# Kernel optimization log

Hardware: AMD Instinct MI355X
Metric: run time of the kernel (lower is better)

Reference implementation:

```python
import jax, jax.numpy as jnp
import numpy as np

NUM_ROUTING = 3


def squash(t, axis=-1):
    # scale * t / ||t||, scale = ||t||^2 / (1 + ||t||^2)  (matches torch code exactly)
    norm = jnp.sum(t * t, axis=axis, keepdims=True)
    return (norm / (1.0 + norm)) * t / jnp.sqrt(norm)


def setup_inputs() -> dict:
    key = jax.random.key(0)
    k1, k2 = jax.random.split(key)
    x = jax.random.normal(k1, (512, 8, 1152), dtype=jnp.float32)      # [B, in_unit, in_channel]
    W = jax.random.normal(k2, (1, 1152, 10, 16, 8), dtype=jnp.float32)  # [1, C, U, unit_size, in_unit]
    return {"x": x, "W": W}


def reference(x, W):
    B = x.shape[0]
    # x.transpose(1,2): [B, C, I];  u_hat = W @ x  -> [B, C, U, O]  (O = unit_size)
    xt = jnp.transpose(x, (0, 2, 1))
    u_hat = jnp.einsum('cuoi,bci->bcuo', W[0], xt)
    # routing logits b_ij, shared across batch: [C, U]
    b = jnp.zeros(u_hat.shape[1:3], dtype=u_hat.dtype)
    v = None
    for _ in range(NUM_ROUTING):
        c = jax.nn.softmax(b, axis=1)                       # softmax over num_unit dim
        s = jnp.einsum('cu,bcuo->buo', c, u_hat)            # sum over in_channel
        v = squash(s, axis=-1)                              # squash over unit_size
        agree = jnp.einsum('bcuo,buo->cu', u_hat, v) / B    # mean over batch
        b = b + agree
    # torch returns v_j.squeeze(1) with trailing singleton -> [B, U, O, 1]
    return v[..., None]
```

## Files before the change

kernel.cpp:

```cpp
#include <hip/hip_runtime.h>
#include <math.h>

#define B_ 512
#define C_ 1152
#define U_ 10
#define O_ 16
#define I_ 8
#define K_ 9216
#define UO_ 160
#define NBLK 256
#define NTHR 1024

typedef short bf16x8 __attribute__((ext_vector_type(8)));
typedef float f32x4 __attribute__((ext_vector_type(4)));
typedef unsigned short u16x8v __attribute__((ext_vector_type(8)));
typedef unsigned long long u64t;

__device__ __attribute__((aligned(16))) unsigned short g_xb2[B_*K_];
__device__ __attribute__((aligned(16))) unsigned short g_xT2[K_*B_];
__device__ __attribute__((aligned(16))) unsigned short g_Wc[3][C_*1280];
__device__ __attribute__((aligned(16))) unsigned g_vT32[2][UO_*B_/2];
__device__ float g_b[C_*U_];
__device__ unsigned g_gen;
__device__ unsigned g_arrive[NBLK];

__device__ __forceinline__ unsigned short f2bf(float f) {
    unsigned u = __builtin_bit_cast(unsigned, f);
    unsigned r = (u + 0x7FFFu + ((u >> 16) & 1u)) >> 16;
    return (unsigned short)r;
}

__device__ __forceinline__ void st_sys16(unsigned short* p, u16x8v v) {
    union { u16x8v v; u64t q[2]; } u; u.v = v;
    __hip_atomic_store((u64t*)p,     u.q[0], __ATOMIC_RELAXED, __HIP_MEMORY_SCOPE_SYSTEM);
    __hip_atomic_store(((u64t*)p)+1, u.q[1], __ATOMIC_RELAXED, __HIP_MEMORY_SCOPE_SYSTEM);
}

__global__ __launch_bounds__(256) void k_prep(const float* __restrict__ x,
                                              const float* __restrict__ W) {
    __shared__ unsigned short lds[32*256];
    int task = blockIdx.x, tid = threadIdx.x;
    if (task < 576) {
        int b0 = (task & 15) * 32;
        int c0 = (task >> 4) * 32;
        int li = tid >> 5, lc = tid & 31;
        for (int rep = 0; rep < 32; rep++) {
            float v = x[(b0+rep)*K_ + li*1152 + c0 + lc];
            lds[rep*256 + ((lc*8+li) ^ ((rep&31)<<3))] = f2bf(v);
        }
        __syncthreads();
        {
            int b = tid >> 3, part = tid & 7;
            int swz = (b&31) << 3;
            const u16x8v* lv = (const u16x8v*)lds;
            u16x8v* ov = (u16x8v*)(g_xb2 + (b0+b)*K_ + c0*8 + part*32);
            #pragma unroll
            for (int g = 0; g < 4; g++)
                ov[g] = lv[(b*256 + ((part*32 + g*8) ^ swz)) >> 3];
        }
        for (int p = 0; p < 8; p++) {
            int r = p*32 + (tid>>3);
            int bp = (tid&7)*4;
            ushort4 o;
            unsigned short* po = (unsigned short*)&o;
            #pragma unroll
            for (int q = 0; q < 4; q++) {
                int b = bp + q;
                po[q] = lds[b*256 + (r ^ ((b&31)<<3))];
            }
            *(ushort4*)(g_xT2 + (c0*8 + r)*B_ + b0 + bp) = o;
        }
    } else {
        int base = (task - 576) * 8192;
        for (int j = 0; j < 8; j++) {
            float4 v = *(const float4*)(W + base + j*1024 + tid*4);
            ushort4 o;
            o.x = f2bf(0.1f*v.x); o.y = f2bf(0.1f*v.y);
            o.z = f2bf(0.1f*v.z); o.w = f2bf(0.1f*v.w);
            *(ushort4*)(&g_Wc[0][0] + base + j*1024 + tid*4) = o;
        }
    }
}

struct TBsh { float agg[2][U_]; float cws[2][U_]; };
union ShMem {
    float red[16][16][32];
    TBsh tb[4];
};

__device__ __forceinline__ void gbar(unsigned target) {
    __syncthreads();
    if (threadIdx.x == 0)
        __hip_atomic_store(&g_arrive[blockIdx.x], target,
                           __ATOMIC_RELAXED, __HIP_MEMORY_SCOPE_SYSTEM);
    if (blockIdx.x == 0) {
        long spins = 0;
        for (;;) {
            int ok = 1;
            if (threadIdx.x < NBLK) {
                unsigned a = __hip_atomic_load(&g_arrive[threadIdx.x],
                                               __ATOMIC_RELAXED, __HIP_MEMORY_SCOPE_SYSTEM);
                ok = (int)(a - target) >= 0;
            }
            if (__syncthreads_count(ok) == NTHR) break;
            __builtin_amdgcn_s_sleep(4);
            if (++spins > (1L << 17)) break;
        }
        if (threadIdx.x == 0)
            __hip_atomic_store(&g_gen, target, __ATOMIC_RELAXED, __HIP_MEMORY_SCOPE_SYSTEM);
    }
    if (threadIdx.x == 0) {
        long spins = 0;
        while ((int)(__hip_atomic_load(&g_gen, __ATOMIC_RELAXED, __HIP_MEMORY_SCOPE_SYSTEM) - target) < 0) {
            __builtin_amdgcn_s_sleep(8);
            if (++spins > (1L << 18)) break;
        }
    }
    __syncthreads();
}

__device__ void ph_s(const unsigned short* __restrict__ Wcr, unsigned* vtw,
                     float* __restrict__ out, int bid, int tid, ShMem& sh) {
    if (bid < 160) {
        int lane = tid & 63, w = tid >> 6;
        int mt = bid & 31, nt = bid >> 5;
        int m0 = mt*16, n0 = nt*32;
        int ra = lane & 15;
        const unsigned short* pa  = g_xb2 + (m0+ra)*K_ + w*576 + (lane>>4)*8;
        const unsigned short* pb0 = Wcr + (w*72 + (lane>>4))*1280 + (n0+ra)*8;
        const unsigned short* pb1 = pb0 + 128;
        f32x4 acc0 = {0.f,0.f,0.f,0.f};
        f32x4 acc1 = {0.f,0.f,0.f,0.f};
        #pragma unroll 6
        for (int s = 0; s < 18; s++) {
            bf16x8 a  = *(const bf16x8*)pa;
            bf16x8 b0 = *(const bf16x8*)pb0;
            bf16x8 b1 = *(const bf16x8*)pb1;
            acc0 = __builtin_amdgcn_mfma_f32_16x16x32_bf16(a, b0, acc0, 0, 0, 0);
            acc1 = __builtin_amdgcn_mfma_f32_16x16x32_bf16(a, b1, acc1, 0, 0, 0);
            pa += 32; pb0 += 5120; pb1 += 5120;
        }
        int row = (lane>>4)*4, col = lane & 15;
        #pragma unroll
        for (int r = 0; r < 4; r++) {
            sh.red[w][row+r][col]    = acc0[r];
            sh.red[w][row+r][col+16] = acc1[r];
        }
        __syncthreads();
        if (tid < 256) {
            int bp = tid >> 5;
            int u  = (tid >> 4) & 1;
            int o  = tid & 15;
            int col2 = u*16 + o;
            float t0 = 0.f, t1 = 0.f;
            #pragma unroll
            for (int ww = 0; ww < 16; ww++) {
                t0 += sh.red[ww][2*bp][col2];
                t1 += sh.red[ww][2*bp+1][col2];
            }
            float n0s = t0*t0, n1s = t1*t1;
            #pragma unroll
            for (int m = 1; m < 16; m <<= 1) {
                n0s += __shfl_xor(n0s, m);
                n1s += __shfl_xor(n1s, m);
            }
            float f0 = n0s / ((1.f + n0s) * sqrtf(n0s));
            float f1 = n1s / ((1.f + n1s) * sqrtf(n1s));
            float v0 = t0*f0, v1 = t1*f1;
            int ug = nt*2 + u;
            int bg = m0 + 2*bp;
            if (vtw) {
                unsigned pack = (unsigned)f2bf(v0) | ((unsigned)f2bf(v1) << 16);
                __hip_atomic_store(&vtw[((ug*16+o)*B_ + bg) >> 1], pack,
                                   __ATOMIC_RELAXED, __HIP_MEMORY_SCOPE_SYSTEM);
            } else {
                out[(bg*10 + ug)*16 + o]       = v0;
                out[((bg+1)*10 + ug)*16 + o]   = v1;
            }
        }
        __syncthreads();
    }
}

__device__ void ph_tb(const float* __restrict__ W, const unsigned* vtr,
                      unsigned short* Wcw, int first, int bid, int tid, ShMem& sh) {
    int lane = tid & 63, lw = (tid >> 6) & 3, g = tid >> 8;
    int ltid = tid & 255;
    int t = bid + 256*g;
    int valid = (t < 576);
    const unsigned short* vT = (const unsigned short*)vtr;
    int c0 = t * 2;
    int ra = lane & 15, kq = (lane>>4)*8;
    int ct = lane >> 5;
    int i0 = ((lane>>4) & 1) * 4;
    int o  = lane & 15;
    if (valid) {
        const unsigned short* pa0 = g_xT2 + (c0*8 + ra)*B_ + kq;
        for (int nt = lw; nt < 5; nt += 4) {
            int n0 = nt*32;
            const unsigned short* pa  = pa0;
            const unsigned short* pb0 = vT + (n0+ra)*B_ + kq;
            const unsigned short* pb1 = pb0 + 16*B_;
            f32x4 acc0 = {0.f,0.f,0.f,0.f};
            f32x4 acc1 = {0.f,0.f,0.f,0.f};
            #pragma unroll 4
            for (int s = 0; s < 16; s++) {
                bf16x8 a  = *(const bf16x8*)pa;
                bf16x8 b0 = *(const bf16x8*)pb0;
                bf16x8 b1 = *(const bf16x8*)pb1;
                acc0 = __builtin_amdgcn_mfma_f32_16x16x32_bf16(a, b0, acc0, 0, 0, 0);
                acc1 = __builtin_amdgcn_mfma_f32_16x16x32_bf16(a, b1, acc1, 0, 0, 0);
                pa += 32; pb0 += 32; pb1 += 32;
            }
            const float* wr = W + (c0+ct)*1280;
            float4 wa = *(const float4*)(wr + (2*nt  )*128 + o*8 + i0);
            float4 wb = *(const float4*)(wr + (2*nt+1)*128 + o*8 + i0);
            float p0 = wa.x*acc0[0] + wa.y*acc0[1] + wa.z*acc0[2] + wa.w*acc0[3];
            float p1 = wb.x*acc1[0] + wb.y*acc1[1] + wb.z*acc1[2] + wb.w*acc1[3];
            #pragma unroll
            for (int m = 1; m < 32; m <<= 1) {
                p0 += __shfl_xor(p0, m);
                p1 += __shfl_xor(p1, m);
            }
            if ((lane & 31) == 0) {
                sh.tb[g].agg[ct][2*nt]   = p0 * (1.f/512.f);
                sh.tb[g].agg[ct][2*nt+1] = p1 * (1.f/512.f);
            }
        }
    }
    __syncthreads();
    if (valid && ltid < 2) {
        int c = c0 + ltid;
        float bv[U_];
        float mx = -3e38f;
        #pragma unroll
        for (int u = 0; u < U_; u++) {
            float v = sh.tb[g].agg[ltid][u];
            if (!first) v += g_b[c*U_ + u];
            g_b[c*U_ + u] = v;
            bv[u] = v;
            mx = fmaxf(mx, v);
        }
        float sm = 0.f;
        #pragma unroll
        for (int u = 0; u < U_; u++) { bv[u] = expf(bv[u] - mx); sm += bv[u]; }
        float inv = 1.f/sm;
        #pragma unroll
        for (int u = 0; u < U_; u++) sh.tb[g].cws[ltid][u] = bv[u]*inv;
    }
    __syncthreads();
    if (valid) {
        for (int e = ltid*8; e < 2560; e += 2048) {
            int ch  = (e >= 1280) ? 1 : 0;
            int off = e - ch*1280;
            int u   = off >> 7;
            float s = sh.tb[g].cws[ch][u];
            const float* wp = W + (c0+ch)*1280 + off;
            float4 a4 = *(const float4*)wp;
            float4 b4 = *(const float4*)(wp + 4);
            u16x8v ov;
            ov[0] = f2bf(a4.x*s); ov[1] = f2bf(a4.y*s); ov[2] = f2bf(a4.z*s); ov[3] = f2bf(a4.w*s);
            ov[4] = f2bf(b4.x*s); ov[5] = f2bf(b4.y*s); ov[6] = f2bf(b4.z*s); ov[7] = f2bf(b4.w*s);
            st_sys16(Wcw + (c0+ch)*1280 + off, ov);
        }
    }
    __syncthreads();
}

__global__ __launch_bounds__(NTHR) void k_mega(const float* __restrict__ W,
                                               float* __restrict__ out) {
    __shared__ ShMem sh;
    __shared__ unsigned sG0;
    int bid = blockIdx.x, tid = threadIdx.x;
    if (tid == 0)
        sG0 = __hip_atomic_load(&g_gen, __ATOMIC_RELAXED, __HIP_MEMORY_SCOPE_SYSTEM);
    __syncthreads();
    unsigned G0 = sG0;
    ph_s(&g_Wc[0][0], &g_vT32[0][0], out, bid, tid, sh);
    gbar(G0 + 1);
    ph_tb(W, &g_vT32[0][0], &g_Wc[1][0], 1, bid, tid, sh);
    gbar(G0 + 2);
    ph_s(&g_Wc[1][0], &g_vT32[1][0], out, bid, tid, sh);
    gbar(G0 + 3);
    ph_tb(W, &g_vT32[1][0], &g_Wc[2][0], 0, bid, tid, sh);
    gbar(G0 + 4);
    ph_s(&g_Wc[2][0], nullptr, out, bid, tid, sh);
}

extern "C" void kernel_launch(void* const* d_in, const int* in_sizes, int n_in,
                              void* d_out, int out_size, void* d_ws, size_t ws_size,
                              hipStream_t stream) {
    const float* x = (const float*)d_in[0];
    const float* W = (const float*)d_in[1];
    float* out = (float*)d_out;
    k_prep<<<dim3(756), dim3(256), 0, stream>>>(x, W);
    k_mega<<<dim3(NBLK), dim3(NTHR), 0, stream>>>(W, out);
}
```

Measured before the change: 123.9 us.

## Apply routing coefficients on the fly instead of materializing scaled W copies

Instead of rewriting a full scaled bf16 copy of W after each routing step, the tb phase now stores only the small softmax coefficient table (U x C). The s-phase GEMM loads the unscaled bf16 W once and multiplies each 8-element fragment by its coefficient in registers before the MFMA, using packed bf16 conversion. Idle blocks in the s-phase also touch x-transpose and W lines to prefetch them into cache for the next tb phase. This removes a large system-scope write per routing iteration, at the cost of extra ALU work and a second rounding step (W is rounded to bf16 before scaling) inside the MFMA loop.

```diff
diff --git a/kernel.cpp b/kernel.cpp
--- a/kernel.cpp
+++ b/kernel.cpp
@@ -18,7 +18,8 @@
 
 __device__ __attribute__((aligned(16))) unsigned short g_xb2[B_*K_];
 __device__ __attribute__((aligned(16))) unsigned short g_xT2[K_*B_];
-__device__ __attribute__((aligned(16))) unsigned short g_Wc[3][C_*1280];
+__device__ __attribute__((aligned(16))) unsigned short g_Wtb[C_*1280];
+__device__ __attribute__((aligned(16))) float g_cwT[3][U_*C_];
 __device__ __attribute__((aligned(16))) unsigned g_vT32[2][UO_*B_/2];
 __device__ float g_b[C_*U_];
 __device__ unsigned g_gen;
@@ -30,10 +31,18 @@
     return (unsigned short)r;
 }
 
-__device__ __forceinline__ void st_sys16(unsigned short* p, u16x8v v) {
-    union { u16x8v v; u64t q[2]; } u; u.v = v;
-    __hip_atomic_store((u64t*)p,     u.q[0], __ATOMIC_RELAXED, __HIP_MEMORY_SCOPE_SYSTEM);
-    __hip_atomic_store(((u64t*)p)+1, u.q[1], __ATOMIC_RELAXED, __HIP_MEMORY_SCOPE_SYSTEM);
+__device__ __forceinline__ bf16x8 scale8(u16x8v w, float s) {
+    bf16x8 r;
+    #pragma unroll
+    for (int p = 0; p < 4; p++) {
+        float lo = __builtin_bit_cast(float, ((unsigned)w[2*p])   << 16) * s;
+        float hi = __builtin_bit_cast(float, ((unsigned)w[2*p+1]) << 16) * s;
+        unsigned pk;
+        asm("v_cvt_pk_bf16_f32 %0, %1, %2" : "=v"(pk) : "v"(lo), "v"(hi));
+        r[2*p]   = (short)(pk & 0xFFFFu);
+        r[2*p+1] = (short)(pk >> 16);
+    }
+    return r;
 }
 
 __global__ __launch_bounds__(256) void k_prep(const float* __restrict__ x,
@@ -70,15 +79,17 @@
             }
             *(ushort4*)(g_xT2 + (c0*8 + r)*B_ + b0 + bp) = o;
         }
-    } else {
+    } else if (task < 756) {
         int base = (task - 576) * 8192;
         for (int j = 0; j < 8; j++) {
             float4 v = *(const float4*)(W + base + j*1024 + tid*4);
             ushort4 o;
-            o.x = f2bf(0.1f*v.x); o.y = f2bf(0.1f*v.y);
-            o.z = f2bf(0.1f*v.z); o.w = f2bf(0.1f*v.w);
-            *(ushort4*)(&g_Wc[0][0] + base + j*1024 + tid*4) = o;
-        }
+            o.x = f2bf(v.x); o.y = f2bf(v.y);
+            o.z = f2bf(v.z); o.w = f2bf(v.w);
+            *(ushort4*)(g_Wtb + base + j*1024 + tid*4) = o;
+        }
+    } else {
+        for (int i = tid; i < U_*C_; i += 256) g_cwT[0][i] = 0.1f;
     }
 }
 
@@ -119,26 +130,32 @@
     __syncthreads();
 }
 
-__device__ void ph_s(const unsigned short* __restrict__ Wcr, unsigned* vtw,
-                     float* __restrict__ out, int bid, int tid, ShMem& sh) {
+__device__ void ph_s(const float* __restrict__ cwv, unsigned* vtw,
+                     const float* __restrict__ W, float* __restrict__ out,
+                     int bid, int tid, ShMem& sh) {
     if (bid < 160) {
         int lane = tid & 63, w = tid >> 6;
         int mt = bid & 31, nt = bid >> 5;
         int m0 = mt*16, n0 = nt*32;
         int ra = lane & 15;
         const unsigned short* pa  = g_xb2 + (m0+ra)*K_ + w*576 + (lane>>4)*8;
-        const unsigned short* pb0 = Wcr + (w*72 + (lane>>4))*1280 + (n0+ra)*8;
-        const unsigned short* pb1 = pb0 + 128;
+        const unsigned short* pw0 = g_Wtb + (w*72 + (lane>>4))*1280 + (n0+ra)*8;
+        const unsigned short* pw1 = pw0 + 128;
+        const float* pc = cwv + (2*nt)*C_ + w*72 + (lane>>4);
         f32x4 acc0 = {0.f,0.f,0.f,0.f};
         f32x4 acc1 = {0.f,0.f,0.f,0.f};
         #pragma unroll 6
         for (int s = 0; s < 18; s++) {
             bf16x8 a  = *(const bf16x8*)pa;
-            bf16x8 b0 = *(const bf16x8*)pb0;
-            bf16x8 b1 = *(const bf16x8*)pb1;
+            u16x8v w0 = *(const u16x8v*)pw0;
+            u16x8v w1 = *(const u16x8v*)pw1;
+            float s0 = pc[0];
+            float s1 = pc[C_];
+            bf16x8 b0 = scale8(w0, s0);
+            bf16x8 b1 = scale8(w1, s1);
             acc0 = __builtin_amdgcn_mfma_f32_16x16x32_bf16(a, b0, acc0, 0, 0, 0);
             acc1 = __builtin_amdgcn_mfma_f32_16x16x32_bf16(a, b1, acc1, 0, 0, 0);
-            pa += 32; pb0 += 5120; pb1 += 5120;
+            pa += 32; pw0 += 5120; pw1 += 5120; pc += 4;
         }
         int row = (lane>>4)*4, col = lane & 15;
         #pragma unroll
@@ -179,11 +196,30 @@
             }
         }
         __syncthreads();
+    } else {
+        float sink = 0.f;
+        #pragma unroll
+        for (int g2 = 0; g2 < 3; g2++) {
+            int t = bid + 256*g2;
+            if (t < 576) {
+                if (tid < 256) {
+                    const float* p = (const float*)((const char*)g_xT2 + t*16384) + tid*16;
+                    sink += *p;
+                }
+                if (tid >= 256 && tid < 416) {
+                    const float* p = W + t*2560 + (tid-256)*16;
+                    sink += *p;
+                }
+            }
+        }
+        asm volatile("" :: "v"(sink));
+        __syncthreads();
+        __syncthreads();
     }
 }
 
 __device__ void ph_tb(const float* __restrict__ W, const unsigned* vtr,
-                      unsigned short* Wcw, int first, int bid, int tid, ShMem& sh) {
+                      float* cww, int first, int bid, int tid, ShMem& sh) {
     int lane = tid & 63, lw = (tid >> 6) & 3, g = tid >> 8;
     int ltid = tid & 255;
     int t = bid + 256*g;
@@ -249,20 +285,10 @@
         for (int u = 0; u < U_; u++) sh.tb[g].cws[ltid][u] = bv[u]*inv;
     }
     __syncthreads();
-    if (valid) {
-        for (int e = ltid*8; e < 2560; e += 2048) {
-            int ch  = (e >= 1280) ? 1 : 0;
-            int off = e - ch*1280;
-            int u   = off >> 7;
-            float s = sh.tb[g].cws[ch][u];
-            const float* wp = W + (c0+ch)*1280 + off;
-            float4 a4 = *(const float4*)wp;
-            float4 b4 = *(const float4*)(wp + 4);
-            u16x8v ov;
-            ov[0] = f2bf(a4.x*s); ov[1] = f2bf(a4.y*s); ov[2] = f2bf(a4.z*s); ov[3] = f2bf(a4.w*s);
-            ov[4] = f2bf(b4.x*s); ov[5] = f2bf(b4.y*s); ov[6] = f2bf(b4.z*s); ov[7] = f2bf(b4.w*s);
-            st_sys16(Wcw + (c0+ch)*1280 + off, ov);
-        }
+    if (valid && ltid < 20) {
+        int u = ltid >> 1, ch = ltid & 1;
+        __hip_atomic_store(&cww[u*C_ + c0 + ch], sh.tb[g].cws[ch][u],
+                           __ATOMIC_RELAXED, __HIP_MEMORY_SCOPE_SYSTEM);
     }
     __syncthreads();
 }
@@ -276,15 +302,15 @@
         sG0 = __hip_atomic_load(&g_gen, __ATOMIC_RELAXED, __HIP_MEMORY_SCOPE_SYSTEM);
     __syncthreads();
     unsigned G0 = sG0;
-    ph_s(&g_Wc[0][0], &g_vT32[0][0], out, bid, tid, sh);
+    ph_s(g_cwT[0], &g_vT32[0][0], W, out, bid, tid, sh);
     gbar(G0 + 1);
-    ph_tb(W, &g_vT32[0][0], &g_Wc[1][0], 1, bid, tid, sh);
+    ph_tb(W, &g_vT32[0][0], g_cwT[1], 1, bid, tid, sh);
     gbar(G0 + 2);
-    ph_s(&g_Wc[1][0], &g_vT32[1][0], out, bid, tid, sh);
+    ph_s(g_cwT[1], &g_vT32[1][0], W, out, bid, tid, sh);
     gbar(G0 + 3);
-    ph_tb(W, &g_vT32[1][0], &g_Wc[2][0], 0, bid, tid, sh);
+    ph_tb(W, &g_vT32[1][0], g_cwT[2], 0, bid, tid, sh);
     gbar(G0 + 4);
-    ph_s(&g_Wc[2][0], nullptr, out, bid, tid, sh);
+    ph_s(g_cwT[2], nullptr, W, out, bid, tid, sh);
 }
 
 extern "C" void kernel_launch(void* const* d_in, const int* in_sizes, int n_in,
@@ -293,6 +319,6 @@
     const float* x = (const float*)d_in[0];
     const float* W = (const float*)d_in[1];
     float* out = (float*)d_out;
-    k_prep<<<dim3(756), dim3(256), 0, stream>>>(x, W);
+    k_prep<<<dim3(757), dim3(256), 0, stream>>>(x, W);
     k_mega<<<dim3(NBLK), dim3(NTHR), 0, stream>>>(W, out);
 }
```

Measured after the change: 127.8 us. +3.2%, slower.
